# Kernel tuning notes

Hardware: AMD Instinct MI355X
Metric: run time of the kernel (lower is better)

Reference implementation:

```python
import jax, jax.numpy as jnp
import numpy as np

N_HEADS = 16
ROPE_BASE = 10000.0


def _rope_tables(T, head_dim, dtype):
    d2 = head_dim // 2
    inv_freq = 1.0 / (ROPE_BASE ** (jnp.arange(0, head_dim, 2, dtype=jnp.float32) / head_dim))
    t = jnp.arange(T, dtype=jnp.float32)
    freqs = jnp.outer(t, inv_freq)  # [T, d2]
    cos = jnp.cos(freqs)[None, :, None, :].astype(dtype)  # [1,T,1,d2]
    sin = jnp.sin(freqs)[None, :, None, :].astype(dtype)
    return cos, sin


def _apply_rotary(x, cos, sin):
    # x: [B,T,H,D]; rotate halves
    d = x.shape[-1] // 2
    x1, x2 = x[..., :d], x[..., d:]
    return jnp.concatenate([x1 * cos + x2 * sin, -x1 * sin + x2 * cos], axis=-1)


def setup_inputs() -> dict:
    key = jax.random.key(0)
    k1, k2, k3 = jax.random.split(key, 3)
    B, T, C = 2, 2048, 1024
    x = jax.random.normal(k1, (B, T, C), dtype=jnp.float32)
    w_attn = jax.random.normal(k2, (3 * C, C), dtype=jnp.float32) * (1.0 / np.sqrt(C))
    w_proj = jax.random.normal(k3, (C, C), dtype=jnp.float32) * (1.0 / np.sqrt(C))
    return {"x": x, "w_attn": w_attn, "w_proj": w_proj}


def reference(x, w_attn, w_proj):
    B, T, C = x.shape
    H = N_HEADS
    D = C // H
    qkv = jnp.einsum('btc,fc->btf', x, w_attn)  # [B,T,3C]
    q, k, v = jnp.split(qkv, 3, axis=2)
    q = q.reshape(B, T, H, D)
    k = k.reshape(B, T, H, D)
    v = v.reshape(B, T, H, D)
    cos, sin = _rope_tables(T, D, x.dtype)
    q = _apply_rotary(q, cos, sin)
    k = _apply_rotary(k, cos, sin)
    # causal SDPA, scale 1/sqrt(D)
    scale = 1.0 / np.sqrt(D)
    scores = jnp.einsum('bqhd,bkhd->bhqk', q, k) * scale
    causal = jnp.tril(jnp.ones((T, T), dtype=bool))
    scores = jnp.where(causal[None, None], scores, jnp.finfo(scores.dtype).min)
    attn = jax.nn.softmax(scores, axis=-1)
    y = jnp.einsum('bhqk,bkhd->bqhd', attn, v).reshape(B, T, C)
    return jnp.einsum('btc,oc->bto', y, w_proj)
```

## Files before the change

kernel.cpp:

```cpp
#include <hip/hip_runtime.h>
#include <math.h>

typedef __bf16 bf16x8 __attribute__((ext_vector_type(8)));
typedef float f32x4 __attribute__((ext_vector_type(4)));

__device__ __forceinline__ unsigned f2bf(float f) {
    union { float f; unsigned u; } v; v.f = f;
    return (v.u + 0x7FFFu + ((v.u >> 16) & 1u)) >> 16;
}

__device__ __forceinline__ void gload16(const ushort* g, ushort* l) {
    __builtin_amdgcn_global_load_lds(
        (const __attribute__((address_space(1))) void*)g,
        (__attribute__((address_space(3))) void*)l, 16, 0, 0);
}

__device__ __forceinline__ bool src_is_fp32(const unsigned* s) {
    int sane = 0;
#pragma unroll
    for (int i = 0; i < 64; ++i) {
        unsigned lo = s[i] & 0xFFFFu;
        unsigned e = (lo >> 7) & 0xFF;
        if (lo == 0u || (e >= 100u && e <= 140u)) sane++;
    }
    return sane < 48;
}

__global__ __launch_bounds__(256) void tobf16_kernel(const unsigned* __restrict__ src,
                                                     ushort* __restrict__ dst, int n) {
    const bool isf32 = src_is_fp32(src);
    int i0 = (blockIdx.x * 256 + threadIdx.x) * 8;
    int stride = gridDim.x * 256 * 8;
    if (isf32) {
        const float* fs = (const float*)src;
        for (int i = i0; i < n; i += stride) {
            float4 f0 = *(const float4*)(fs + i);
            float4 f1 = *(const float4*)(fs + i + 4);
            uint4 o;
            o.x = f2bf(f0.x) | (f2bf(f0.y) << 16);
            o.y = f2bf(f0.z) | (f2bf(f0.w) << 16);
            o.z = f2bf(f1.x) | (f2bf(f1.y) << 16);
            o.w = f2bf(f1.z) | (f2bf(f1.w) << 16);
            *(uint4*)(dst + i) = o;
        }
    } else {
        const ushort* us = (const ushort*)src;
        for (int i = i0; i < n; i += stride)
            *(uint4*)(dst + i) = *(const uint4*)(us + i);
    }
}

constexpr int GBM = 128, GBN = 128, GBK = 32;

__global__ __launch_bounds__(256) void gemm_qkv_rope_kernel(
    const ushort* __restrict__ A, const ushort* __restrict__ Bmat,
    ushort* __restrict__ qkvh, int K) {
    __shared__ ushort As[GBM * GBK];
    __shared__ ushort Bs[GBN * GBK];

    const int tid  = threadIdx.x;
    const int lane = tid & 63;
    const int wv   = tid >> 6;
    const int wm   = (wv >> 1) * 64;
    const int wn   = (wv & 1) * 64;

    const ushort* Ab = A + (size_t)blockIdx.x * GBM * K;
    const ushort* Bb = Bmat + (size_t)blockIdx.y * GBN * K;

    f32x4 acc[4][4];
#pragma unroll
    for (int i = 0; i < 4; i++)
#pragma unroll
        for (int j = 0; j < 4; j++) acc[i][j] = (f32x4){0.f, 0.f, 0.f, 0.f};

    const int srow = tid >> 2;
    const int scol = (tid & 3) * 8;
    const int fr = lane & 15;
    const int fk = (lane >> 4) * 8;
    ushort* adst = As + wv * 512;
    ushort* bdst = Bs + wv * 512;

    for (int k0 = 0; k0 < K; k0 += GBK) {
        __syncthreads();
        gload16(Ab + (size_t)srow * K + k0 + scol,        adst);
        gload16(Ab + (size_t)(srow + 64) * K + k0 + scol, adst + 2048);
        gload16(Bb + (size_t)srow * K + k0 + scol,        bdst);
        gload16(Bb + (size_t)(srow + 64) * K + k0 + scol, bdst + 2048);
        __syncthreads();

        bf16x8 af[4], bfr[4];
#pragma unroll
        for (int i = 0; i < 4; i++)
            af[i] = *(const bf16x8*)(As + (wm + i * 16 + fr) * GBK + fk);
#pragma unroll
        for (int j = 0; j < 4; j++)
            bfr[j] = *(const bf16x8*)(Bs + (wn + j * 16 + fr) * GBK + fk);
#pragma unroll
        for (int i = 0; i < 4; i++)
#pragma unroll
            for (int j = 0; j < 4; j++)
                acc[i][j] = __builtin_amdgcn_mfma_f32_16x16x32_bf16(af[i], bfr[j], acc[i][j], 0, 0, 0);
    }

    const int crow0 = (lane >> 4) * 4;
    const int col0  = blockIdx.y * GBN + wn;
    const int which = col0 >> 10;
    const int hh    = (col0 >> 6) & 15;
    ushort* outp = qkvh + (size_t)which * 4194304 + (size_t)hh * 131072;

    if (which < 2) {
        const float inva = exp2f((float)fr * -0.41524101186f);
        const float invb = exp2f((float)(fr + 16) * -0.41524101186f);
        const float qs = (which == 0) ? 0.125f : 1.0f;
#pragma unroll
        for (int i = 0; i < 4; i++)
#pragma unroll
            for (int r = 0; r < 4; r++) {
                int row = blockIdx.x * GBM + wm + i * 16 + crow0 + r;
                int t = row & 2047;
                size_t ob = ((size_t)(row >> 11)) * 2097152 + (size_t)t * 64;
                float sa, ca, sb, cb;
                __sincosf((float)t * inva, &sa, &ca);
                __sincosf((float)t * invb, &sb, &cb);
                float q0 = acc[i][0][r], q1 = acc[i][1][r];
                float q2 = acc[i][2][r], q3 = acc[i][3][r];
                float n0 = (q0 * ca + q2 * sa) * qs;
                float n1 = (q1 * cb + q3 * sb) * qs;
                float n2 = (q2 * ca - q0 * sa) * qs;
                float n3 = (q3 * cb - q1 * sb) * qs;
                outp[ob + fr]      = (ushort)f2bf(n0);
                outp[ob + 16 + fr] = (ushort)f2bf(n1);
                outp[ob + 32 + fr] = (ushort)f2bf(n2);
                outp[ob + 48 + fr] = (ushort)f2bf(n3);
            }
    } else {
#pragma unroll
        for (int i = 0; i < 4; i++)
#pragma unroll
            for (int r = 0; r < 4; r++) {
                int row = blockIdx.x * GBM + wm + i * 16 + crow0 + r;
                int t = row & 2047;
                size_t ob = ((size_t)(row >> 11)) * 2097152 + (size_t)t * 64;
#pragma unroll
                for (int j = 0; j < 4; j++)
                    outp[ob + j * 16 + fr] = (ushort)f2bf(acc[i][j][r]);
            }
    }
}

__global__ __launch_bounds__(256) void gemm_bt_kernel(
    const ushort* __restrict__ A, const ushort* __restrict__ Bmat,
    float* __restrict__ C, int M, int N, int K) {
    __shared__ ushort As[GBM * GBK];
    __shared__ ushort Bs[GBN * GBK];

    const int tid  = threadIdx.x;
    const int lane = tid & 63;
    const int wv   = tid >> 6;
    const int wm   = (wv >> 1) * 64;
    const int wn   = (wv & 1) * 64;

    const ushort* Ab = A + (size_t)blockIdx.x * GBM * K;
    const ushort* Bb = Bmat + (size_t)blockIdx.y * GBN * K;

    f32x4 acc[4][4];
#pragma unroll
    for (int i = 0; i < 4; i++)
#pragma unroll
        for (int j = 0; j < 4; j++) acc[i][j] = (f32x4){0.f, 0.f, 0.f, 0.f};

    const int srow = tid >> 2;
    const int scol = (tid & 3) * 8;
    const int fr = lane & 15;
    const int fk = (lane >> 4) * 8;
    ushort* adst = As + wv * 512;
    ushort* bdst = Bs + wv * 512;

    for (int k0 = 0; k0 < K; k0 += GBK) {
        __syncthreads();
        gload16(Ab + (size_t)srow * K + k0 + scol,        adst);
        gload16(Ab + (size_t)(srow + 64) * K + k0 + scol, adst + 2048);
        gload16(Bb + (size_t)srow * K + k0 + scol,        bdst);
        gload16(Bb + (size_t)(srow + 64) * K + k0 + scol, bdst + 2048);
        __syncthreads();

        bf16x8 af[4], bfr[4];
#pragma unroll
        for (int i = 0; i < 4; i++)
            af[i] = *(const bf16x8*)(As + (wm + i * 16 + fr) * GBK + fk);
#pragma unroll
        for (int j = 0; j < 4; j++)
            bfr[j] = *(const bf16x8*)(Bs + (wn + j * 16 + fr) * GBK + fk);
#pragma unroll
        for (int i = 0; i < 4; i++)
#pragma unroll
            for (int j = 0; j < 4; j++)
                acc[i][j] = __builtin_amdgcn_mfma_f32_16x16x32_bf16(af[i], bfr[j], acc[i][j], 0, 0, 0);
    }

    const int crow0 = (lane >> 4) * 4;
#pragma unroll
    for (int i = 0; i < 4; i++)
#pragma unroll
        for (int j = 0; j < 4; j++)
#pragma unroll
            for (int r = 0; r < 4; r++) {
                int row = blockIdx.x * GBM + wm + i * 16 + crow0 + r;
                int col = blockIdx.y * GBN + wn + j * 16 + fr;
                C[(size_t)row * N + col] = acc[i][j][r];
            }
}

#define NEG_BIG (-1e30f)
constexpr int LPK = 72;
constexpr int LPV = 136;

__global__ __launch_bounds__(512) void attn_kernel(const ushort* __restrict__ qkvh,
                                                   ushort* __restrict__ y) {
    __shared__ ushort smem[26112];
    ushort* Ks = smem;
    ushort* Ps = smem;
    ushort* Vt = smem + 17408;

    const int tid  = threadIdx.x;
    const int lane = tid & 63;
    const int wv   = tid >> 6;
    const int pid  = blockIdx.x;
    const int bh   = blockIdx.y;
    const int b    = bh >> 4, h = bh & 15;

    const ushort* qp = qkvh + (size_t)b * 2097152 + (size_t)h * 131072;
    const ushort* kp = qp + 4194304;
    const ushort* vp = qp + 8388608;

    const int fr = lane & 15;
    const int fq = lane >> 4;
    const int fk = fq * 8;

    const int srow = tid >> 2;
    const int scol = (tid & 3) * 16;
    const int vkey = tid & 127;
    const int vd0  = (tid >> 7) * 16;

#pragma unroll 1
    for (int seg = 0; seg < 2; ++seg) {
        const int qb = seg ? (15 - pid) : pid;
        const int nIt = qb + 1;

        const int qrow = qb * 128 + wv * 16 + fr;
        bf16x8 qf0 = *(const bf16x8*)(qp + (size_t)qrow * 64 + fk);
        bf16x8 qf1 = *(const bf16x8*)(qp + (size_t)qrow * 64 + 32 + fk);

        f32x4 o[4];
        o[0] = o[1] = o[2] = o[3] = (f32x4){0.f, 0.f, 0.f, 0.f};
        float lacc[4] = {0.f, 0.f, 0.f, 0.f};

        uint4 kr0, kr1, vr0, vr1;
        {
            const ushort* sk = kp + (size_t)tid * 16;
            kr0 = *(const uint4*)(sk);
            kr1 = *(const uint4*)(sk + 8);
            const ushort* sv = vp + (size_t)vkey * 64 + vd0;
            vr0 = *(const uint4*)(sv);
            vr1 = *(const uint4*)(sv + 8);
        }

#pragma unroll 1
        for (int it = 0; it < nIt; ++it) {
            const int k0 = it * 128;
            __syncthreads();
            *(uint4*)(Ks + srow * LPK + scol)     = kr0;
            *(uint4*)(Ks + srow * LPK + scol + 8) = kr1;
            {
                unsigned w[8] = {vr0.x, vr0.y, vr0.z, vr0.w, vr1.x, vr1.y, vr1.z, vr1.w};
#pragma unroll
                for (int jj = 0; jj < 8; ++jj) {
                    Vt[(vd0 + 2 * jj)     * LPV + vkey] = (ushort)(w[jj] & 0xFFFFu);
                    Vt[(vd0 + 2 * jj + 1) * LPV + vkey] = (ushort)(w[jj] >> 16);
                }
            }
            if (it + 1 < nIt) {
                const ushort* sk = kp + (size_t)(k0 + 128) * 64 + (size_t)tid * 16;
                kr0 = *(const uint4*)(sk);
                kr1 = *(const uint4*)(sk + 8);
                const ushort* sv = vp + (size_t)(k0 + 128 + vkey) * 64 + vd0;
                vr0 = *(const uint4*)(sv);
                vr1 = *(const uint4*)(sv + 8);
            }
            __syncthreads();

            f32x4 s[8];
#pragma unroll
            for (int j = 0; j < 8; ++j) {
                bf16x8 kf0 = *(const bf16x8*)(Ks + (j * 16 + fr) * LPK + fk);
                bf16x8 kf1 = *(const bf16x8*)(Ks + (j * 16 + fr) * LPK + 32 + fk);
                f32x4 z = (f32x4){0.f, 0.f, 0.f, 0.f};
                z = __builtin_amdgcn_mfma_f32_16x16x32_bf16(qf0, kf0, z, 0, 0, 0);
                z = __builtin_amdgcn_mfma_f32_16x16x32_bf16(qf1, kf1, z, 0, 0, 0);
                s[j] = z;
            }
            if (it < qb) {
#pragma unroll
                for (int j = 0; j < 8; ++j)
#pragma unroll
                    for (int r = 0; r < 4; ++r) {
                        float p = __expf(s[j][r]);
                        s[j][r] = p;
                        lacc[r] += p;
                    }
            } else {
                const int rowg = qb * 128 + wv * 16 + fq * 4;
#pragma unroll
                for (int j = 0; j < 8; ++j)
#pragma unroll
                    for (int r = 0; r < 4; ++r) {
                        float v = s[j][r];
                        if ((k0 + j * 16 + fr) > (rowg + r)) v = NEG_BIG;
                        float p = __expf(v);
                        s[j][r] = p;
                        lacc[r] += p;
                    }
            }

            __syncthreads();
            ushort* pw = Ps + wv * (16 * LPV);
#pragma unroll
            for (int j = 0; j < 8; ++j)
#pragma unroll
                for (int r = 0; r < 4; ++r)
                    pw[(fq * 4 + r) * LPV + j * 16 + fr] = (ushort)f2bf(s[j][r]);
            __syncthreads();

#pragma unroll
            for (int kk = 0; kk < 4; ++kk) {
                bf16x8 pf = *(const bf16x8*)(pw + fr * LPV + kk * 32 + fk);
#pragma unroll
                for (int j = 0; j < 4; ++j) {
                    bf16x8 vf = *(const bf16x8*)(Vt + (j * 16 + fr) * LPV + kk * 32 + fk);
                    o[j] = __builtin_amdgcn_mfma_f32_16x16x32_bf16(pf, vf, o[j], 0, 0, 0);
                }
            }
        }

#pragma unroll
        for (int msk = 1; msk < 16; msk <<= 1)
#pragma unroll
            for (int r = 0; r < 4; ++r)
                lacc[r] += __shfl_xor(lacc[r], msk, 64);
#pragma unroll
        for (int j = 0; j < 4; ++j)
#pragma unroll
            for (int r = 0; r < 4; ++r) {
                int row = qb * 128 + wv * 16 + fq * 4 + r;
                y[((size_t)b * 2048 + row) * 1024 + h * 64 + j * 16 + fr] =
                    (ushort)f2bf(o[j][r] / lacc[r]);
            }
    }
}

extern "C" void kernel_launch(void* const* d_in, const int* in_sizes, int n_in,
                              void* d_out, int out_size, void* d_ws, size_t ws_size,
                              hipStream_t stream) {
    const int nx = in_sizes[0];
    const int na = in_sizes[1];
    const int np = in_sizes[2];

    ushort* qkvh = (ushort*)d_ws;
    ushort* yb   = qkvh + (size_t)3 * 4194304;
    ushort* xb   = yb + (size_t)4096 * 1024;
    ushort* wab  = xb + nx;
    ushort* wpb  = wab + na;
    size_t need = ((size_t)3 * 4194304 + (size_t)4096 * 1024 + nx + na + np) * 2;
    if (ws_size < need) return;

    tobf16_kernel<<<dim3(1024), 256, 0, stream>>>((const unsigned*)d_in[0], xb, nx);
    tobf16_kernel<<<dim3(1024), 256, 0, stream>>>((const unsigned*)d_in[1], wab, na);
    tobf16_kernel<<<dim3(512),  256, 0, stream>>>((const unsigned*)d_in[2], wpb, np);

    gemm_qkv_rope_kernel<<<dim3(32, 24), 256, 0, stream>>>(xb, wab, qkvh, 1024);
    attn_kernel<<<dim3(8, 32), 512, 0, stream>>>(qkvh, yb);
    gemm_bt_kernel<<<dim3(32, 8), 256, 0, stream>>>(yb, wpb, (float*)d_out, 4096, 1024, 1024);
}
```

Before: 203.3 us.

## Merge bf16 conversions into one launch and shrink attention query tiles to 64

The three fp32-to-bf16 conversion launches become one kernel that dispatches on block index, with one block per 2048 elements and no grid-stride loop. The attention kernel moves from 128-query tiles with 512 threads to 64-query tiles with 256 threads. This doubles the grid to 16x32 blocks for better CU occupancy and gives each wave a private P buffer, which removes two block barriers per iteration. In exchange, each 128-key K/V tile is loaded for only 64 queries, so K/V traffic per query rises, and the diagonal tile is masked over more wasted work.

Result: no change. 204.9 us (+0.8%).

```diff
diff --git a/kernel.cpp b/kernel.cpp
--- a/kernel.cpp
+++ b/kernel.cpp
@@ -26,27 +26,30 @@
     return sane < 48;
 }
 
-__global__ __launch_bounds__(256) void tobf16_kernel(const unsigned* __restrict__ src,
-                                                     ushort* __restrict__ dst, int n) {
-    const bool isf32 = src_is_fp32(src);
-    int i0 = (blockIdx.x * 256 + threadIdx.x) * 8;
-    int stride = gridDim.x * 256 * 8;
-    if (isf32) {
+__global__ __launch_bounds__(256) void tobf16_all_kernel(
+    const unsigned* __restrict__ s0, const unsigned* __restrict__ s1,
+    const unsigned* __restrict__ s2,
+    ushort* __restrict__ d0, ushort* __restrict__ d1, ushort* __restrict__ d2) {
+    const int bx = blockIdx.x;
+    const unsigned* src;
+    ushort* dst;
+    int lb;
+    if (bx < 2048)      { src = s0; dst = d0; lb = bx; }
+    else if (bx < 3584) { src = s1; dst = d1; lb = bx - 2048; }
+    else                { src = s2; dst = d2; lb = bx - 3584; }
+    const int i = lb * 2048 + threadIdx.x * 8;
+    if (src_is_fp32(src)) {
         const float* fs = (const float*)src;
-        for (int i = i0; i < n; i += stride) {
-            float4 f0 = *(const float4*)(fs + i);
-            float4 f1 = *(const float4*)(fs + i + 4);
-            uint4 o;
-            o.x = f2bf(f0.x) | (f2bf(f0.y) << 16);
-            o.y = f2bf(f0.z) | (f2bf(f0.w) << 16);
-            o.z = f2bf(f1.x) | (f2bf(f1.y) << 16);
-            o.w = f2bf(f1.z) | (f2bf(f1.w) << 16);
-            *(uint4*)(dst + i) = o;
-        }
+        float4 f0 = *(const float4*)(fs + i);
+        float4 f1 = *(const float4*)(fs + i + 4);
+        uint4 o;
+        o.x = f2bf(f0.x) | (f2bf(f0.y) << 16);
+        o.y = f2bf(f0.z) | (f2bf(f0.w) << 16);
+        o.z = f2bf(f1.x) | (f2bf(f1.y) << 16);
+        o.w = f2bf(f1.z) | (f2bf(f1.w) << 16);
+        *(uint4*)(dst + i) = o;
     } else {
-        const ushort* us = (const ushort*)src;
-        for (int i = i0; i < n; i += stride)
-            *(uint4*)(dst + i) = *(const uint4*)(us + i);
+        *(uint4*)(dst + i) = *(const uint4*)((const ushort*)src + i);
     }
 }
 
@@ -215,12 +218,11 @@
 constexpr int LPK = 72;
 constexpr int LPV = 136;
 
-__global__ __launch_bounds__(512) void attn_kernel(const ushort* __restrict__ qkvh,
+__global__ __launch_bounds__(256) void attn_kernel(const ushort* __restrict__ qkvh,
                                                    ushort* __restrict__ y) {
-    __shared__ ushort smem[26112];
-    ushort* Ks = smem;
-    ushort* Ps = smem;
-    ushort* Vt = smem + 17408;
+    __shared__ ushort Ks[128 * LPK];
+    __shared__ ushort Vt[64 * LPV];
+    __shared__ ushort Ps[4][16 * LPV];
 
     const int tid  = threadIdx.x;
     const int lane = tid & 63;
@@ -237,17 +239,17 @@
     const int fq = lane >> 4;
     const int fk = fq * 8;
 
-    const int srow = tid >> 2;
-    const int scol = (tid & 3) * 16;
+    const int srow = tid >> 1;
+    const int scol = (tid & 1) * 32;
     const int vkey = tid & 127;
-    const int vd0  = (tid >> 7) * 16;
+    const int vd0  = (tid >> 7) * 32;
 
 #pragma unroll 1
     for (int seg = 0; seg < 2; ++seg) {
-        const int qb = seg ? (15 - pid) : pid;
-        const int nIt = qb + 1;
-
-        const int qrow = qb * 128 + wv * 16 + fr;
+        const int qb = seg ? (31 - pid) : pid;
+        const int nIt = (qb + 2) >> 1;
+
+        const int qrow = qb * 64 + wv * 16 + fr;
         bf16x8 qf0 = *(const bf16x8*)(qp + (size_t)qrow * 64 + fk);
         bf16x8 qf1 = *(const bf16x8*)(qp + (size_t)qrow * 64 + 32 + fk);
 
@@ -255,39 +257,50 @@
         o[0] = o[1] = o[2] = o[3] = (f32x4){0.f, 0.f, 0.f, 0.f};
         float lacc[4] = {0.f, 0.f, 0.f, 0.f};
 
-        uint4 kr0, kr1, vr0, vr1;
+        uint4 kr0, kr1, kr2, kr3, vr0, vr1, vr2, vr3;
         {
-            const ushort* sk = kp + (size_t)tid * 16;
+            const ushort* sk = kp + (size_t)srow * 64 + scol;
             kr0 = *(const uint4*)(sk);
             kr1 = *(const uint4*)(sk + 8);
+            kr2 = *(const uint4*)(sk + 16);
+            kr3 = *(const uint4*)(sk + 24);
             const ushort* sv = vp + (size_t)vkey * 64 + vd0;
             vr0 = *(const uint4*)(sv);
             vr1 = *(const uint4*)(sv + 8);
+            vr2 = *(const uint4*)(sv + 16);
+            vr3 = *(const uint4*)(sv + 24);
         }
 
 #pragma unroll 1
         for (int it = 0; it < nIt; ++it) {
             const int k0 = it * 128;
             __syncthreads();
-            *(uint4*)(Ks + srow * LPK + scol)     = kr0;
-            *(uint4*)(Ks + srow * LPK + scol + 8) = kr1;
+            *(uint4*)(Ks + srow * LPK + scol)      = kr0;
+            *(uint4*)(Ks + srow * LPK + scol + 8)  = kr1;
+            *(uint4*)(Ks + srow * LPK + scol + 16) = kr2;
+            *(uint4*)(Ks + srow * LPK + scol + 24) = kr3;
             {
-                unsigned w[8] = {vr0.x, vr0.y, vr0.z, vr0.w, vr1.x, vr1.y, vr1.z, vr1.w};
-#pragma unroll
-                for (int jj = 0; jj < 8; ++jj) {
+                unsigned w[16] = {vr0.x, vr0.y, vr0.z, vr0.w, vr1.x, vr1.y, vr1.z, vr1.w,
+                                  vr2.x, vr2.y, vr2.z, vr2.w, vr3.x, vr3.y, vr3.z, vr3.w};
+#pragma unroll
+                for (int jj = 0; jj < 16; ++jj) {
                     Vt[(vd0 + 2 * jj)     * LPV + vkey] = (ushort)(w[jj] & 0xFFFFu);
                     Vt[(vd0 + 2 * jj + 1) * LPV + vkey] = (ushort)(w[jj] >> 16);
                 }
             }
+            __syncthreads();
             if (it + 1 < nIt) {
-                const ushort* sk = kp + (size_t)(k0 + 128) * 64 + (size_t)tid * 16;
+                const ushort* sk = kp + (size_t)(k0 + 128 + srow) * 64 + scol;
                 kr0 = *(const uint4*)(sk);
                 kr1 = *(const uint4*)(sk + 8);
+                kr2 = *(const uint4*)(sk + 16);
+                kr3 = *(const uint4*)(sk + 24);
                 const ushort* sv = vp + (size_t)(k0 + 128 + vkey) * 64 + vd0;
                 vr0 = *(const uint4*)(sv);
                 vr1 = *(const uint4*)(sv + 8);
-            }
-            __syncthreads();
+                vr2 = *(const uint4*)(sv + 16);
+                vr3 = *(const uint4*)(sv + 24);
+            }
 
             f32x4 s[8];
 #pragma unroll
@@ -299,7 +312,7 @@
                 z = __builtin_amdgcn_mfma_f32_16x16x32_bf16(qf1, kf1, z, 0, 0, 0);
                 s[j] = z;
             }
-            if (it < qb) {
+            if (it + 1 < nIt) {
 #pragma unroll
                 for (int j = 0; j < 8; ++j)
 #pragma unroll
@@ -309,7 +322,7 @@
                         lacc[r] += p;
                     }
             } else {
-                const int rowg = qb * 128 + wv * 16 + fq * 4;
+                const int rowg = qb * 64 + wv * 16 + fq * 4;
 #pragma unroll
                 for (int j = 0; j < 8; ++j)
 #pragma unroll
@@ -322,14 +335,13 @@
                     }
             }
 
-            __syncthreads();
-            ushort* pw = Ps + wv * (16 * LPV);
+            ushort* pw = Ps[wv];
 #pragma unroll
             for (int j = 0; j < 8; ++j)
 #pragma unroll
                 for (int r = 0; r < 4; ++r)
                     pw[(fq * 4 + r) * LPV + j * 16 + fr] = (ushort)f2bf(s[j][r]);
-            __syncthreads();
+            __asm__ volatile("" ::: "memory");
 
 #pragma unroll
             for (int kk = 0; kk < 4; ++kk) {
@@ -351,7 +363,7 @@
         for (int j = 0; j < 4; ++j)
 #pragma unroll
             for (int r = 0; r < 4; ++r) {
-                int row = qb * 128 + wv * 16 + fq * 4 + r;
+                int row = qb * 64 + wv * 16 + fq * 4 + r;
                 y[((size_t)b * 2048 + row) * 1024 + h * 64 + j * 16 + fr] =
                     (ushort)f2bf(o[j][r] / lacc[r]);
             }
@@ -373,11 +385,11 @@
     size_t need = ((size_t)3 * 4194304 + (size_t)4096 * 1024 + nx + na + np) * 2;
     if (ws_size < need) return;
 
-    tobf16_kernel<<<dim3(1024), 256, 0, stream>>>((const unsigned*)d_in[0], xb, nx);
-    tobf16_kernel<<<dim3(1024), 256, 0, stream>>>((const unsigned*)d_in[1], wab, na);
-    tobf16_kernel<<<dim3(512),  256, 0, stream>>>((const unsigned*)d_in[2], wpb, np);
+    tobf16_all_kernel<<<dim3(4096), 256, 0, stream>>>(
+        (const unsigned*)d_in[0], (const unsigned*)d_in[1], (const unsigned*)d_in[2],
+        xb, wab, wpb);
 
     gemm_qkv_rope_kernel<<<dim3(32, 24), 256, 0, stream>>>(xb, wab, qkvh, 1024);
-    attn_kernel<<<dim3(8, 32), 512, 0, stream>>>(qkvh, yb);
+    attn_kernel<<<dim3(16, 32), 256, 0, stream>>>(qkvh, yb);
     gemm_bt_kernel<<<dim3(32, 8), 256, 0, stream>>>(yb, wpb, (float*)d_out, 4096, 1024, 1024);
 }
```
